# Kernel tuning notes

Hardware: AMD Instinct MI355X
Metric: run time of the kernel (lower is better)

The kernel has to match this reference:

```python
import itertools
import jax, jax.numpy as jnp
import numpy as np

B, O, E = 4096, 8, 64        # batch, num objects, latent dim
I, V = 4, 3                  # max_invariants, max_variables
PERM_IDXS = np.array(list(itertools.permutations(range(O), V)), dtype=np.int32)  # [P, V], P = 8*7*6 = 336


def setup_inputs() -> dict:
    key = jax.random.key(0)
    k1, k2, k3, k4 = jax.random.split(key, 4)
    return {
        "unary_feats": jax.random.normal(k1, (B, O, E), dtype=jnp.float32),
        "binary_feats": jax.random.normal(k2, (B, O, O, E), dtype=jnp.float32),
        # learned weights (RandomNormal(mean=0) in the original, stddev 0.05 default)
        "rule_unary": jax.random.normal(k3, (I, V, E), dtype=jnp.float32) * 0.05,
        "rule_binary": jax.random.normal(k4, (I, V, V, E), dtype=jnp.float32) * 0.05,
    }


def reference(unary_feats, binary_feats, rule_unary, rule_binary):
    perm = jnp.asarray(PERM_IDXS)  # [P, V]
    # unary_match[b,i,k,l] = sum_e unary_feats[b,l,e] * rule_unary[i,k,e]
    unary_match = jnp.einsum('ble,ike->bikl', unary_feats, rule_unary)  # [B, I, V, O]
    # gather: unary_perm_scores[b,i,p,v] = unary_match[b,i,v,perm[p,v]]
    v_idx = jnp.arange(V)[None, :]                      # [1, V]
    unary_perm_scores = unary_match[:, :, v_idx, perm]  # [B, I, P, V]
    unary_scores = unary_perm_scores.sum(-1)            # [B, I, P]

    # binary_match[b,i,n,m,j,k] = sum_e binary_feats[b,j,k,e] * rule_binary[i,n,m,e]
    binary_match = jnp.einsum('bjke,inme->binmjk', binary_feats, rule_binary)  # [B, I, V, V, O, O]
    # gather per permutation: scores[b,i,p,n,m] = binary_match[b,i,n,m,perm[p,n],perm[p,m]]
    n = jnp.arange(V)[None, :, None]  # [1, V, 1]
    m = jnp.arange(V)[None, None, :]  # [1, 1, V]
    pn = perm[:, :, None]             # [P, V, 1]
    pm = perm[:, None, :]             # [P, 1, V]
    binary_perm_scores = binary_match[:, :, n, m, pn, pm]  # [B, I, P, V, V]
    binary_scores = binary_perm_scores.sum((-1, -2))        # [B, I, P]

    merged_scores = (unary_scores + binary_scores).min(-1)  # [B, I] (min over permutations)
    inv_select = jax.nn.softmax(merged_scores, axis=-1)     # [B, I]
    rule_labels = jax.nn.one_hot(jnp.array([0, 0, 1, 1]), 4, dtype=inv_select.dtype)  # [4, 4]
    return inv_select @ rule_labels                          # [B, 4]
```

## Files before the change

### kernel.cpp

```cpp
#include <hip/hip_runtime.h>
#include <math.h>


typedef __attribute__((ext_vector_type(8))) __bf16 bf16x8;
typedef __attribute__((ext_vector_type(4))) float  f32x4;

#define QS 68
#define SS 12

__device__ inline bf16x8 cvt2(const float4 v0, const float4 v1) {
    bf16x8 r;
    r[0] = (__bf16)v0.x; r[1] = (__bf16)v0.y; r[2] = (__bf16)v0.z; r[3] = (__bf16)v0.w;
    r[4] = (__bf16)v1.x; r[5] = (__bf16)v1.y; r[6] = (__bf16)v1.z; r[7] = (__bf16)v1.w;
    return r;
}

__global__ __launch_bounds__(64, 2) void rule_learner_kernel(
    const float* __restrict__ uf,
    const float* __restrict__ bfe,
    const float* __restrict__ ru,
    const float* __restrict__ rb,
    float* __restrict__ out)
{
    const int b0    = blockIdx.x * 2;
    const int lane  = threadIdx.x;
    const int row16 = lane & 15;
    const int kg    = lane >> 4;
    const int kb    = kg * 8;

    __shared__ float q_s [12 * QS];
    __shared__ float q2_s[12 * QS];
    __shared__ float ss_s[12 * SS];

    const int cc16  = row16 < 12 ? row16 : 11;
    const int ii    = cc16 / 3, tt = cc16 - ii * 3;
    const int rule1 = ii * 9 + (tt == 0 ? 1 : tt == 1 ? 2 : 5);
    const int rule2 = ii * 9 + (tt == 0 ? 3 : tt == 1 ? 6 : 7);
    const int ruled = ii * 9 + tt * 4;
    bf16x8 b1f0, b1f1, b2f0, b2f1, dbf0, dbf1, ruf0, ruf1;
    {
        const float* r1 = rb + rule1 * 64 + kb;
        b1f0 = cvt2(*(const float4*)r1,        *(const float4*)(r1 + 4));
        b1f1 = cvt2(*(const float4*)(r1 + 32), *(const float4*)(r1 + 36));
        const float* r2 = rb + rule2 * 64 + kb;
        b2f0 = cvt2(*(const float4*)r2,        *(const float4*)(r2 + 4));
        b2f1 = cvt2(*(const float4*)(r2 + 32), *(const float4*)(r2 + 36));
        const float* rd = rb + ruled * 64 + kb;
        dbf0 = cvt2(*(const float4*)rd,        *(const float4*)(rd + 4));
        dbf1 = cvt2(*(const float4*)(rd + 32), *(const float4*)(rd + 36));
        const float* rr = ru + cc16 * 64 + kb;
        ruf0 = cvt2(*(const float4*)rr,        *(const float4*)(rr + 4));
        ruf1 = cvt2(*(const float4*)(rr + 32), *(const float4*)(rr + 36));
    }

    float4 af[4][4], uA[4], dA[4];
    {
        const float* base = bfe + (size_t)b0 * 4096;
        #pragma unroll
        for (int t = 0; t < 4; ++t) {
            const float* rp = base + (size_t)(t * 16 + row16) * 64 + kb;
            af[t][0] = *(const float4*)rp;
            af[t][1] = *(const float4*)(rp + 4);
            af[t][2] = *(const float4*)(rp + 32);
            af[t][3] = *(const float4*)(rp + 36);
        }
        const int v8c = row16 < 8 ? row16 : 7;
        const float* up = uf + (size_t)b0 * 512 + v8c * 64 + kb;
        uA[0] = *(const float4*)up;        uA[1] = *(const float4*)(up + 4);
        uA[2] = *(const float4*)(up + 32); uA[3] = *(const float4*)(up + 36);
        const float* dp = base + v8c * 576 + kb;
        dA[0] = *(const float4*)dp;        dA[1] = *(const float4*)(dp + 4);
        dA[2] = *(const float4*)(dp + 32); dA[3] = *(const float4*)(dp + 36);
    }

    #pragma unroll
    for (int e = 0; e < 2; ++e) {
        f32x4 g1[4];
        #pragma unroll
        for (int t = 0; t < 4; ++t) {
            const bf16x8 a0 = cvt2(af[t][0], af[t][1]);
            const bf16x8 a1 = cvt2(af[t][2], af[t][3]);
            f32x4 z1 = {0.f, 0.f, 0.f, 0.f};
            z1 = __builtin_amdgcn_mfma_f32_16x16x32_bf16(a0, b1f0, z1, 0, 0, 0);
            z1 = __builtin_amdgcn_mfma_f32_16x16x32_bf16(a1, b1f1, z1, 0, 0, 0);
            g1[t] = z1;
            f32x4 z2 = {0.f, 0.f, 0.f, 0.f};
            z2 = __builtin_amdgcn_mfma_f32_16x16x32_bf16(a0, b2f0, z2, 0, 0, 0);
            z2 = __builtin_amdgcn_mfma_f32_16x16x32_bf16(a1, b2f1, z2, 0, 0, 0);
            if (row16 < 12)
                *(float4*)&q2_s[row16 * QS + t * 16 + kg * 4] = *(float4*)&z2;
        }
        {
            const bf16x8 ua0 = cvt2(uA[0], uA[1]);
            const bf16x8 ua1 = cvt2(uA[2], uA[3]);
            const bf16x8 da0 = cvt2(dA[0], dA[1]);
            const bf16x8 da1 = cvt2(dA[2], dA[3]);
            f32x4 zs = {0.f, 0.f, 0.f, 0.f};
            zs = __builtin_amdgcn_mfma_f32_16x16x32_bf16(ua0, ruf0, zs, 0, 0, 0);
            zs = __builtin_amdgcn_mfma_f32_16x16x32_bf16(ua1, ruf1, zs, 0, 0, 0);
            zs = __builtin_amdgcn_mfma_f32_16x16x32_bf16(da0, dbf0, zs, 0, 0, 0);
            zs = __builtin_amdgcn_mfma_f32_16x16x32_bf16(da1, dbf1, zs, 0, 0, 0);
            if (row16 < 12 && kg < 2)
                *(float4*)&ss_s[row16 * SS + kg * 4] = *(float4*)&zs;
        }

        if (e == 0) {
            const float* base = bfe + (size_t)(b0 + 1) * 4096;
            #pragma unroll
            for (int t = 0; t < 4; ++t) {
                const float* rp = base + (size_t)(t * 16 + row16) * 64 + kb;
                af[t][0] = *(const float4*)rp;
                af[t][1] = *(const float4*)(rp + 4);
                af[t][2] = *(const float4*)(rp + 32);
                af[t][3] = *(const float4*)(rp + 36);
            }
            const int v8c = row16 < 8 ? row16 : 7;
            const float* up = uf + (size_t)(b0 + 1) * 512 + v8c * 64 + kb;
            uA[0] = *(const float4*)up;        uA[1] = *(const float4*)(up + 4);
            uA[2] = *(const float4*)(up + 32); uA[3] = *(const float4*)(up + 36);
            const float* dp = base + v8c * 576 + kb;
            dA[0] = *(const float4*)dp;        dA[1] = *(const float4*)(dp + 4);
            dA[2] = *(const float4*)(dp + 32); dA[3] = *(const float4*)(dp + 36);
        }

        if (row16 < 12) {
            #pragma unroll
            for (int t = 0; t < 4; ++t) {
                const int p0 = t * 16 + kg * 4;
                float4 add;
                {
                    const int p = p0 + 0, rv = ((p & 7) << 3) | (p >> 3);
                    add.x = q2_s[row16 * QS + rv];
                }
                {
                    const int p = p0 + 1, rv = ((p & 7) << 3) | (p >> 3);
                    add.y = q2_s[row16 * QS + rv];
                }
                {
                    const int p = p0 + 2, rv = ((p & 7) << 3) | (p >> 3);
                    add.z = q2_s[row16 * QS + rv];
                }
                {
                    const int p = p0 + 3, rv = ((p & 7) << 3) | (p >> 3);
                    add.w = q2_s[row16 * QS + rv];
                }
                float4 res;
                res.x = g1[t][0] + add.x; res.y = g1[t][1] + add.y;
                res.z = g1[t][2] + add.z; res.w = g1[t][3] + add.w;
                *(float4*)&q_s[row16 * QS + p0] = res;
            }
        }

        float mn[4] = {INFINITY, INFINITY, INFINITY, INFINITY};
        if (lane < 56) {
            const int a  = lane / 7;
            const int o  = lane - a * 7;
            const int bb = o + (o >= a);
            #pragma unroll
            for (int i = 0; i < 4; ++i) {
                const float bs = q_s[(i * 3 + 0) * QS + a * 8 + bb]
                               + ss_s[(i * 3 + 0) * SS + a]
                               + ss_s[(i * 3 + 1) * SS + bb];
                const float4 c0 = *(const float4*)&q_s[(i * 3 + 1) * QS + a * 8];
                const float4 c1 = *(const float4*)&q_s[(i * 3 + 1) * QS + a * 8 + 4];
                const float4 d0 = *(const float4*)&q_s[(i * 3 + 2) * QS + bb * 8];
                const float4 d1 = *(const float4*)&q_s[(i * 3 + 2) * QS + bb * 8 + 4];
                const float4 e0 = *(const float4*)&ss_s[(i * 3 + 2) * SS];
                const float4 e1 = *(const float4*)&ss_s[(i * 3 + 2) * SS + 4];
                float vv[8];
                vv[0] = c0.x + d0.x + e0.x; vv[1] = c0.y + d0.y + e0.y;
                vv[2] = c0.z + d0.z + e0.z; vv[3] = c0.w + d0.w + e0.w;
                vv[4] = c1.x + d1.x + e1.x; vv[5] = c1.y + d1.y + e1.y;
                vv[6] = c1.z + d1.z + e1.z; vv[7] = c1.w + d1.w + e1.w;
                float m = INFINITY;
                #pragma unroll
                for (int cc = 0; cc < 8; ++cc) {
                    const float s = (cc == a || cc == bb) ? INFINITY : (bs + vv[cc]);
                    m = fminf(m, s);
                }
                mn[i] = m;
            }
        }
        #pragma unroll
        for (int s = 1; s <= 32; s <<= 1) {
            #pragma unroll
            for (int i = 0; i < 4; ++i) mn[i] = fminf(mn[i], __shfl_xor(mn[i], s));
        }
        if (lane == 0) {
            const float mx = fmaxf(fmaxf(mn[0], mn[1]), fmaxf(mn[2], mn[3]));
            const float e0 = expf(mn[0] - mx), e1 = expf(mn[1] - mx);
            const float e2 = expf(mn[2] - mx), e3 = expf(mn[3] - mx);
            const float inv = 1.f / (e0 + e1 + e2 + e3);
            *(float4*)(out + (size_t)(b0 + e) * 4) =
                make_float4((e0 + e1) * inv, (e2 + e3) * inv, 0.f, 0.f);
        }

        if (e == 0) {
            asm volatile("s_waitcnt lgkmcnt(0)" ::: "memory");
            __builtin_amdgcn_sched_barrier(0);
        }
    }
}

extern "C" void kernel_launch(void* const* d_in, const int* in_sizes, int n_in,
                              void* d_out, int out_size, void* d_ws, size_t ws_size,
                              hipStream_t stream) {
    const float* uf = (const float*)d_in[0];
    const float* bf = (const float*)d_in[1];
    const float* ru = (const float*)d_in[2];
    const float* rb = (const float*)d_in[3];
    float* out = (float*)d_out;

    const int B = in_sizes[0] / (8 * 64);
    rule_learner_kernel<<<B / 2, 64, 0, stream>>>(uf, bf, ru, rb, out);
}
```

Baseline: 21.44 us.

## Fuse transposed binary contribution into MFMA accumulation via transposed global loads

Instead of writing the second rule product to shared memory and re-reading it transposed to add to the first, the kernel now loads the transposed binary-feature rows directly from global memory and accumulates both products in one MFMA chain. Shared buffers are double-buffered per batch element, which removes the explicit LDS wait and sched barrier between the two elements. This drops an LDS round trip and a gather pass. In exchange it doubles global loads of binary features, with strided reads that will mostly hit cache, and uses more registers.

New measurement: 27.14 us. 26.6% more time.

```diff
diff --git a/kernel.cpp b/kernel.cpp
--- a/kernel.cpp
+++ b/kernel.cpp
@@ -28,9 +28,8 @@
     const int kg    = lane >> 4;
     const int kb    = kg * 8;
 
-    __shared__ float q_s [12 * QS];
-    __shared__ float q2_s[12 * QS];
-    __shared__ float ss_s[12 * SS];
+    __shared__ float q_s [2][12 * QS];
+    __shared__ float ss_s[2][12 * SS];
 
     const int cc16  = row16 < 12 ? row16 : 11;
     const int ii    = cc16 / 3, tt = cc16 - ii * 3;
@@ -53,16 +52,16 @@
         ruf1 = cvt2(*(const float4*)(rr + 32), *(const float4*)(rr + 36));
     }
 
-    float4 af[4][4], uA[4], dA[4];
+    float4 afF[4][4], uA[4], dA[4];
     {
         const float* base = bfe + (size_t)b0 * 4096;
         #pragma unroll
         for (int t = 0; t < 4; ++t) {
             const float* rp = base + (size_t)(t * 16 + row16) * 64 + kb;
-            af[t][0] = *(const float4*)rp;
-            af[t][1] = *(const float4*)(rp + 4);
-            af[t][2] = *(const float4*)(rp + 32);
-            af[t][3] = *(const float4*)(rp + 36);
+            afF[t][0] = *(const float4*)rp;
+            afF[t][1] = *(const float4*)(rp + 4);
+            afF[t][2] = *(const float4*)(rp + 32);
+            afF[t][3] = *(const float4*)(rp + 36);
         }
         const int v8c = row16 < 8 ? row16 : 7;
         const float* up = uf + (size_t)b0 * 512 + v8c * 64 + kb;
@@ -74,21 +73,29 @@
     }
 
     #pragma unroll
-    for (int e = 0; e < 2; ++e) {
-        f32x4 g1[4];
+    for (int el = 0; el < 2; ++el) {
+        const float* base = bfe + (size_t)(b0 + el) * 4096;
+
         #pragma unroll
         for (int t = 0; t < 4; ++t) {
-            const bf16x8 a0 = cvt2(af[t][0], af[t][1]);
-            const bf16x8 a1 = cvt2(af[t][2], af[t][3]);
-            f32x4 z1 = {0.f, 0.f, 0.f, 0.f};
-            z1 = __builtin_amdgcn_mfma_f32_16x16x32_bf16(a0, b1f0, z1, 0, 0, 0);
-            z1 = __builtin_amdgcn_mfma_f32_16x16x32_bf16(a1, b1f1, z1, 0, 0, 0);
-            g1[t] = z1;
-            f32x4 z2 = {0.f, 0.f, 0.f, 0.f};
-            z2 = __builtin_amdgcn_mfma_f32_16x16x32_bf16(a0, b2f0, z2, 0, 0, 0);
-            z2 = __builtin_amdgcn_mfma_f32_16x16x32_bf16(a1, b2f1, z2, 0, 0, 0);
+            const int x = t * 2 + (row16 >> 3);
+            const int y = row16 & 7;
+            const float* rp = base + (size_t)(y * 8 + x) * 64 + kb;
+            const float4 r0 = *(const float4*)rp;
+            const float4 r1 = *(const float4*)(rp + 4);
+            const float4 r2 = *(const float4*)(rp + 32);
+            const float4 r3 = *(const float4*)(rp + 36);
+            const bf16x8 aF0 = cvt2(afF[t][0], afF[t][1]);
+            const bf16x8 aF1 = cvt2(afF[t][2], afF[t][3]);
+            const bf16x8 aR0 = cvt2(r0, r1);
+            const bf16x8 aR1 = cvt2(r2, r3);
+            f32x4 acc = {0.f, 0.f, 0.f, 0.f};
+            acc = __builtin_amdgcn_mfma_f32_16x16x32_bf16(aF0, b1f0, acc, 0, 0, 0);
+            acc = __builtin_amdgcn_mfma_f32_16x16x32_bf16(aF1, b1f1, acc, 0, 0, 0);
+            acc = __builtin_amdgcn_mfma_f32_16x16x32_bf16(aR0, b2f0, acc, 0, 0, 0);
+            acc = __builtin_amdgcn_mfma_f32_16x16x32_bf16(aR1, b2f1, acc, 0, 0, 0);
             if (row16 < 12)
-                *(float4*)&q2_s[row16 * QS + t * 16 + kg * 4] = *(float4*)&z2;
+                *(float4*)&q_s[el][row16 * QS + t * 16 + kg * 4] = *(float4*)&acc;
         }
         {
             const bf16x8 ua0 = cvt2(uA[0], uA[1]);
@@ -101,54 +108,26 @@
             zs = __builtin_amdgcn_mfma_f32_16x16x32_bf16(da0, dbf0, zs, 0, 0, 0);
             zs = __builtin_amdgcn_mfma_f32_16x16x32_bf16(da1, dbf1, zs, 0, 0, 0);
             if (row16 < 12 && kg < 2)
-                *(float4*)&ss_s[row16 * SS + kg * 4] = *(float4*)&zs;
+                *(float4*)&ss_s[el][row16 * SS + kg * 4] = *(float4*)&zs;
         }
 
-        if (e == 0) {
-            const float* base = bfe + (size_t)(b0 + 1) * 4096;
+        if (el == 0) {
+            const float* nb = bfe + (size_t)(b0 + 1) * 4096;
             #pragma unroll
             for (int t = 0; t < 4; ++t) {
-                const float* rp = base + (size_t)(t * 16 + row16) * 64 + kb;
-                af[t][0] = *(const float4*)rp;
-                af[t][1] = *(const float4*)(rp + 4);
-                af[t][2] = *(const float4*)(rp + 32);
-                af[t][3] = *(const float4*)(rp + 36);
+                const float* rp = nb + (size_t)(t * 16 + row16) * 64 + kb;
+                afF[t][0] = *(const float4*)rp;
+                afF[t][1] = *(const float4*)(rp + 4);
+                afF[t][2] = *(const float4*)(rp + 32);
+                afF[t][3] = *(const float4*)(rp + 36);
             }
             const int v8c = row16 < 8 ? row16 : 7;
             const float* up = uf + (size_t)(b0 + 1) * 512 + v8c * 64 + kb;
             uA[0] = *(const float4*)up;        uA[1] = *(const float4*)(up + 4);
             uA[2] = *(const float4*)(up + 32); uA[3] = *(const float4*)(up + 36);
-            const float* dp = base + v8c * 576 + kb;
+            const float* dp = nb + v8c * 576 + kb;
             dA[0] = *(const float4*)dp;        dA[1] = *(const float4*)(dp + 4);
             dA[2] = *(const float4*)(dp + 32); dA[3] = *(const float4*)(dp + 36);
-        }
-
-        if (row16 < 12) {
-            #pragma unroll
-            for (int t = 0; t < 4; ++t) {
-                const int p0 = t * 16 + kg * 4;
-                float4 add;
-                {
-                    const int p = p0 + 0, rv = ((p & 7) << 3) | (p >> 3);
-                    add.x = q2_s[row16 * QS + rv];
-                }
-                {
-                    const int p = p0 + 1, rv = ((p & 7) << 3) | (p >> 3);
-                    add.y = q2_s[row16 * QS + rv];
-                }
-                {
-                    const int p = p0 + 2, rv = ((p & 7) << 3) | (p >> 3);
-                    add.z = q2_s[row16 * QS + rv];
-                }
-                {
-                    const int p = p0 + 3, rv = ((p & 7) << 3) | (p >> 3);
-                    add.w = q2_s[row16 * QS + rv];
-                }
-                float4 res;
-                res.x = g1[t][0] + add.x; res.y = g1[t][1] + add.y;
-                res.z = g1[t][2] + add.z; res.w = g1[t][3] + add.w;
-                *(float4*)&q_s[row16 * QS + p0] = res;
-            }
         }
 
         float mn[4] = {INFINITY, INFINITY, INFINITY, INFINITY};
@@ -158,15 +137,15 @@
             const int bb = o + (o >= a);
             #pragma unroll
             for (int i = 0; i < 4; ++i) {
-                const float bs = q_s[(i * 3 + 0) * QS + a * 8 + bb]
-                               + ss_s[(i * 3 + 0) * SS + a]
-                               + ss_s[(i * 3 + 1) * SS + bb];
-                const float4 c0 = *(const float4*)&q_s[(i * 3 + 1) * QS + a * 8];
-                const float4 c1 = *(const float4*)&q_s[(i * 3 + 1) * QS + a * 8 + 4];
-                const float4 d0 = *(const float4*)&q_s[(i * 3 + 2) * QS + bb * 8];
-                const float4 d1 = *(const float4*)&q_s[(i * 3 + 2) * QS + bb * 8 + 4];
-                const float4 e0 = *(const float4*)&ss_s[(i * 3 + 2) * SS];
-                const float4 e1 = *(const float4*)&ss_s[(i * 3 + 2) * SS + 4];
+                const float bs = q_s[el][(i * 3 + 0) * QS + a * 8 + bb]
+                               + ss_s[el][(i * 3 + 0) * SS + a]
+                               + ss_s[el][(i * 3 + 1) * SS + bb];
+                const float4 c0 = *(const float4*)&q_s[el][(i * 3 + 1) * QS + a * 8];
+                const float4 c1 = *(const float4*)&q_s[el][(i * 3 + 1) * QS + a * 8 + 4];
+                const float4 d0 = *(const float4*)&q_s[el][(i * 3 + 2) * QS + bb * 8];
+                const float4 d1 = *(const float4*)&q_s[el][(i * 3 + 2) * QS + bb * 8 + 4];
+                const float4 e0 = *(const float4*)&ss_s[el][(i * 3 + 2) * SS];
+                const float4 e1 = *(const float4*)&ss_s[el][(i * 3 + 2) * SS + 4];
                 float vv[8];
                 vv[0] = c0.x + d0.x + e0.x; vv[1] = c0.y + d0.y + e0.y;
                 vv[2] = c0.z + d0.z + e0.z; vv[3] = c0.w + d0.w + e0.w;
@@ -191,13 +170,8 @@
             const float e0 = expf(mn[0] - mx), e1 = expf(mn[1] - mx);
             const float e2 = expf(mn[2] - mx), e3 = expf(mn[3] - mx);
             const float inv = 1.f / (e0 + e1 + e2 + e3);
-            *(float4*)(out + (size_t)(b0 + e) * 4) =
+            *(float4*)(out + (size_t)(b0 + el) * 4) =
                 make_float4((e0 + e1) * inv, (e2 + e3) * inv, 0.f, 0.f);
-        }
-
-        if (e == 0) {
-            asm volatile("s_waitcnt lgkmcnt(0)" ::: "memory");
-            __builtin_amdgcn_sched_barrier(0);
         }
     }
 }
```
